# Performance work log

Hardware: AMD Instinct MI355X
Metric: run time of the kernel (lower is better)

## Reference

```python
import jax, jax.numpy as jnp
import numpy as np

B, D, H, Z, E = 2048, 1024, 1024, 256, 64


def setup_inputs() -> dict:
    key = jax.random.key(0)
    ks = jax.random.split(key, 16)
    s = lambda k, shape, std=0.02: jax.random.normal(k, shape, dtype=jnp.float32) * std
    return {
        "x": jax.random.normal(ks[0], (B, D), dtype=jnp.float32),
        "h0": jax.random.normal(ks[1], (B, H), dtype=jnp.float32),
        "c0": jax.random.normal(ks[2], (B, H), dtype=jnp.float32),
        "hhat0": jax.random.normal(ks[3], (B, Z), dtype=jnp.float32),
        "chat0": jax.random.normal(ks[4], (B, Z), dtype=jnp.float32),
        "hweight": s(ks[5], (Z + H + D, 4 * Z)),
        "hbias": jnp.zeros((4 * Z,), jnp.float32),
        "zweight_h": s(ks[6], (Z, 4 * E), 0.01),
        "zweight_x": s(ks[7], (Z, 4 * E), 0.01),
        "zweight_b": s(ks[8], (Z, 4 * E), 0.01),
        "zbias_h": jnp.ones((4 * E,), jnp.float32),
        "zbias_x": jnp.ones((4 * E,), jnp.float32),
        # stacked in gate order (i, g, f, o), matching the torch cat order
        "dweight_h": jnp.full((4, E, H), 0.1 / E, jnp.float32),
        "dweight_x": jnp.full((4, E, H), 0.1 / E, jnp.float32),
        "dweight_b": s(ks[9], (4, E, H), 0.01),
        "weight": s(ks[10], (H + D, 4 * H)),
        "bias": jnp.zeros((4 * H,), jnp.float32),
    }


def reference(x, h0, c0, hhat0, chat0, hweight, hbias,
              zweight_h, zweight_x, zweight_b, zbias_h, zbias_x,
              dweight_h, dweight_x, dweight_b, weight, bias):
    # ---- hyper LSTM cell ----
    hcat = jnp.concatenate([hhat0, h0, x], axis=1)                 # [B, Z+H+D]
    hg = hcat @ hweight + hbias                                    # [B, 4Z]
    i_h, g_h, f_h, o_h = jnp.split(hg, 4, axis=1)
    chat1 = jax.nn.sigmoid(f_h) * chat0 + jax.nn.sigmoid(i_h) * jnp.tanh(g_h)
    hhat1 = jax.nn.sigmoid(o_h) * jnp.tanh(chat1)                  # [B, Z]

    # ---- embeddings z (gate order i, g, f, o) ----
    z_h = (hhat1 @ zweight_h + zbias_h).reshape(-1, 4, E)          # [B,4,E]
    z_x = (hhat1 @ zweight_x + zbias_x).reshape(-1, 4, E)
    z_b = (hhat1 @ zweight_b).reshape(-1, 4, E)

    # ---- per-gate modulation vectors d_y* : [B,4,H] -> [B,4H] ----
    d_yh = jnp.einsum('bge,geh->bgh', z_h, dweight_h).reshape(-1, 4 * H)
    d_yx = jnp.einsum('bge,geh->bgh', z_x, dweight_x).reshape(-1, 4 * H)
    d_yb = jnp.einsum('bge,geh->bgh', z_b, dweight_b).reshape(-1, 4 * H)

    # ---- main LSTM with hypernetwork modulation ----
    gates = jnp.concatenate([h0, x], axis=1) @ weight              # [B, 4H]
    gates = gates * d_yh * d_yx + d_yb + bias
    i_g, g_g, f_g, o_g = jnp.split(gates, 4, axis=1)
    c1 = jax.nn.sigmoid(f_g) * c0 + jax.nn.sigmoid(i_g) * jnp.tanh(g_g)
    h1 = jax.nn.sigmoid(o_g) * jnp.tanh(c1)
    return (h1, c1, hhat1, chat1)
```

## Files before the change

### kernel.cpp

```cpp
#include <hip/hip_runtime.h>
#include <hip/hip_bf16.h>
#include <math.h>


typedef __attribute__((ext_vector_type(8))) short bf16x8;
typedef __attribute__((ext_vector_type(4))) float f32x4;
typedef unsigned short u16;

__device__ __forceinline__ u16 f2b(float f) {
  union { float f; unsigned u; } v; v.f = f;
  unsigned r = v.u + 0x7fffu + ((v.u >> 16) & 1u);
  return (u16)(r >> 16);
}
__device__ __forceinline__ float b2f(u16 b) {
  union { unsigned u; float f; } v; v.u = ((unsigned)b) << 16; return v.f;
}
__device__ __forceinline__ float sigm(float x) { return 1.f / (1.f + __expf(-x)); }

#define GLL16(gsrc, ldst)                                                      \
  __builtin_amdgcn_global_load_lds(                                            \
      (const __attribute__((address_space(1))) void*)(gsrc),                   \
      (__attribute__((address_space(3))) void*)(ldst), 16, 0, 0)

__global__ void k_prep(const float* __restrict__ hhat0, const float* __restrict__ h0,
                       const float* __restrict__ x, const float* __restrict__ weight,
                       const float* __restrict__ hweight,
                       const float* __restrict__ zw_h, const float* __restrict__ zw_x,
                       const float* __restrict__ zw_b, const float* __restrict__ dw_h,
                       const float* __restrict__ dw_x, const float* __restrict__ dw_b,
                       u16* __restrict__ hcatb, u16* __restrict__ bt,
                       u16* __restrict__ zwT, u16* __restrict__ dwT) {
  __shared__ float tile[32][66];
  int bid = blockIdx.x;
  const int t = threadIdx.x;
  if (bid < 4608) {
    int i = bid * 256 + t;
    int b = i / 576, c4 = i % 576;
    const float* src;
    if (c4 < 64)       src = hhat0 + (long)b * 256 + c4 * 4;
    else if (c4 < 320) src = h0 + (long)b * 1024 + (c4 - 64) * 4;
    else               src = x + (long)b * 1024 + (c4 - 320) * 4;
    float4 v = *(const float4*)src;
    ushort4 o = {f2b(v.x), f2b(v.y), f2b(v.z), f2b(v.w)};
    *(ushort4*)&hcatb[(long)b * 2304 + c4 * 4] = o;
    return;
  }
  bid -= 4608;
  if (bid < 5760) {
    const int n0 = (bid % 160) * 32, k0 = (bid / 160) * 64;
    if (n0 < 4096 && k0 < 256) return;
    const float* src; int C, sc0, sr0;
    if (n0 >= 4096) { src = hweight; C = 1024; sc0 = n0 - 4096; sr0 = k0; }
    else            { src = weight;  C = 4096; sc0 = n0;        sr0 = k0 - 256; }
    #pragma unroll
    for (int p = 0; p < 8; ++p) {
      int c = t & 31, r = (t >> 5) + 8 * p;
      tile[c][r] = src[(long)(sr0 + r) * C + sc0 + c];
    }
    __syncthreads();
    #pragma unroll
    for (int p = 0; p < 2; ++p) {
      int kc = t & 15, cl = (t >> 4) + 16 * p;
      ushort4 o = {f2b(tile[cl][4 * kc]), f2b(tile[cl][4 * kc + 1]),
                   f2b(tile[cl][4 * kc + 2]), f2b(tile[cl][4 * kc + 3])};
      *(ushort4*)&bt[(long)(n0 + cl) * 2304 + k0 + 4 * kc] = o;
    }
    return;
  }
  bid -= 5760;
  const int zi = bid >> 5, bx = bid & 31;
  const float* src; u16* dst; int R, C;
  if (zi < 3) {
    src = (zi == 0) ? zw_h : (zi == 1) ? zw_x : zw_b;
    dst = zwT + (long)zi * 65536; R = 256; C = 256;
  } else {
    int s = zi - 3, tt = s >> 2, g = s & 3;
    src = ((tt == 0) ? dw_h : (tt == 1) ? dw_x : dw_b) + (long)g * 65536;
    dst = dwT + (long)s * 65536; R = 64; C = 1024;
  }
  const int nct = C / 32;
  const int c0 = (bx % nct) * 32, r0 = (bx / nct) * 64;
  #pragma unroll
  for (int p = 0; p < 8; ++p) {
    int c = t & 31, r = (t >> 5) + 8 * p;
    tile[c][r] = src[(long)(r0 + r) * C + c0 + c];
  }
  __syncthreads();
  #pragma unroll
  for (int p = 0; p < 2; ++p) {
    int kc = t & 15, cl = (t >> 4) + 16 * p;
    ushort4 o = {f2b(tile[cl][4 * kc]), f2b(tile[cl][4 * kc + 1]),
                 f2b(tile[cl][4 * kc + 2]), f2b(tile[cl][4 * kc + 3])};
    *(ushort4*)&dst[(long)(c0 + cl) * R + r0 + 4 * kc] = o;
  }
}

__global__ __launch_bounds__(512, 4)
void k_gemm_main(const u16* __restrict__ A, const u16* __restrict__ Bt,
                 float* __restrict__ hgbuf, u16* __restrict__ grawb) {
  constexpr int K = 2304, BK = 64;
  __shared__ __align__(16) u16 sA[128 * BK];
  __shared__ __align__(16) u16 sB[128 * BK];
  const int m0 = blockIdx.y * 128, n0 = blockIdx.x * 128;
  const int kstart = (n0 < 4096) ? 256 : 0;
  const int tid = threadIdx.x, wave = tid >> 6, lane = tid & 63;
  const int quad = lane >> 4, lrow = lane & 15;
  const int wm = (wave >> 2) * 64, wn = (wave & 3) * 32;

  const int la = tid * 16;
  const int rowa = la >> 7, qa = (((la >> 4) & 7) - rowa) & 7;
  const int lb = 8192 + tid * 16;
  const int rowb = lb >> 7, qb = (((lb >> 4) & 7) - rowb) & 7;
  const long aoff0 = ((long)(m0 + rowa) * K + qa * 8) * 2;
  const long aoff1 = ((long)(m0 + rowb) * K + qb * 8) * 2;
  const long boff0 = ((long)(n0 + rowa) * K + qa * 8) * 2;
  const long boff1 = ((long)(n0 + rowb) * K + qb * 8) * 2;

  const f32x4 vz = {0.f, 0.f, 0.f, 0.f};
  f32x4 acc[4][2];
  #pragma unroll
  for (int i = 0; i < 4; ++i)
    #pragma unroll
    for (int j = 0; j < 2; ++j) acc[i][j] = vz;

  for (int k0 = kstart; k0 < K; k0 += BK) {
    GLL16((const char*)A + aoff0 + (long)k0 * 2, (char*)sA + wave * 1024);
    GLL16((const char*)A + aoff1 + (long)k0 * 2, (char*)sA + 8192 + wave * 1024);
    GLL16((const char*)Bt + boff0 + (long)k0 * 2, (char*)sB + wave * 1024);
    GLL16((const char*)Bt + boff1 + (long)k0 * 2, (char*)sB + 8192 + wave * 1024);
    __syncthreads();

    bf16x8 af[4][2], bf[2][2];
    #pragma unroll
    for (int i = 0; i < 4; ++i) {
      int row = wm + i * 16 + lrow;
      const char* base = (const char*)sA + row * 128;
      af[i][0] = *(const bf16x8*)(base + (((quad + row) & 7) << 4));
      af[i][1] = *(const bf16x8*)(base + (((4 + quad + row) & 7) << 4));
    }
    #pragma unroll
    for (int j = 0; j < 2; ++j) {
      int row = wn + j * 16 + lrow;
      const char* base = (const char*)sB + row * 128;
      bf[j][0] = *(const bf16x8*)(base + (((quad + row) & 7) << 4));
      bf[j][1] = *(const bf16x8*)(base + (((4 + quad + row) & 7) << 4));
    }
    #pragma unroll
    for (int kk = 0; kk < 2; ++kk)
      #pragma unroll
      for (int i = 0; i < 4; ++i)
        #pragma unroll
        for (int j = 0; j < 2; ++j)
          acc[i][j] = __builtin_amdgcn_mfma_f32_16x16x32_bf16(af[i][kk], bf[j][kk], acc[i][j], 0, 0, 0);
    __syncthreads();
  }

  #pragma unroll
  for (int i = 0; i < 4; ++i) {
    #pragma unroll
    for (int j = 0; j < 2; ++j) {
      #pragma unroll
      for (int r = 0; r < 4; ++r) {
        int row = m0 + wm + i * 16 + quad * 4 + r;
        int col = n0 + wn + j * 16 + lrow;
        float v = acc[i][j][r];
        if (col < 4096) grawb[(long)row * 4096 + col] = f2b(v);
        else            hgbuf[(long)row * 1024 + (col - 4096)] = v;
      }
    }
  }
}

__global__ __launch_bounds__(256, 2)
void k_gemm_z(const u16* __restrict__ A, const u16* __restrict__ Bt,
              const float* __restrict__ zbh, const float* __restrict__ zbx,
              u16* __restrict__ zbout) {
  constexpr int K = 256, BK = 32;
  __shared__ __align__(16) u16 sA[64 * BK];
  __shared__ __align__(16) u16 sB[128 * BK];
  const int m0 = blockIdx.y * 64, n0 = blockIdx.x * 128;
  const int tid = threadIdx.x, wave = tid >> 6, lane = tid & 63;
  const int quad = lane >> 4, lrow = lane & 15;
  const int wm = (wave >> 1) * 32, wn = (wave & 1) * 64;

  const int sl = tid * 16;
  const int arow = sl >> 6;
  const int aq = (((sl & 63) >> 4) - (arow >> 1)) & 3;
  const long aoff = ((long)(m0 + arow) * K) * 2 + aq * 16;

  const f32x4 vz = {0.f, 0.f, 0.f, 0.f};
  f32x4 acc[2][4];
  #pragma unroll
  for (int i = 0; i < 2; ++i)
    #pragma unroll
    for (int j = 0; j < 4; ++j) acc[i][j] = vz;

  for (int k0 = 0; k0 < K; k0 += BK) {
    GLL16((const char*)A + aoff + (long)k0 * 2, (char*)sA + wave * 1024);
    #pragma unroll
    for (int c = 0; c < 2; ++c) {
      int l = c * 4096 + sl;
      int row = l >> 6;
      int q = (((l & 63) >> 4) - (row >> 1)) & 3;
      const char* g = (const char*)Bt + ((long)(n0 + row) * K + k0) * 2 + q * 16;
      GLL16(g, (char*)sB + c * 4096 + wave * 1024);
    }
    __syncthreads();
    bf16x8 af[2], bf[4];
    #pragma unroll
    for (int i = 0; i < 2; ++i) {
      int row = wm + i * 16 + lrow;
      af[i] = *(const bf16x8*)((const char*)sA + row * 64 + (((quad + (row >> 1)) & 3) << 4));
    }
    #pragma unroll
    for (int j = 0; j < 4; ++j) {
      int row = wn + j * 16 + lrow;
      bf[j] = *(const bf16x8*)((const char*)sB + row * 64 + (((quad + (row >> 1)) & 3) << 4));
    }
    #pragma unroll
    for (int i = 0; i < 2; ++i)
      #pragma unroll
      for (int j = 0; j < 4; ++j)
        acc[i][j] = __builtin_amdgcn_mfma_f32_16x16x32_bf16(af[i], bf[j], acc[i][j], 0, 0, 0);
    __syncthreads();
  }
  #pragma unroll
  for (int i = 0; i < 2; ++i) {
    #pragma unroll
    for (int j = 0; j < 4; ++j) {
      #pragma unroll
      for (int r = 0; r < 4; ++r) {
        int row = m0 + wm + i * 16 + quad * 4 + r;
        int col = n0 + wn + j * 16 + lrow;
        float v = acc[i][j][r] + ((col < 256) ? zbh[col] : (col < 512) ? zbx[col - 256] : 0.f);
        zbout[(long)row * 768 + col] = f2b(v);
      }
    }
  }
}

__global__ void k_hyper_act(const float* __restrict__ hgbuf, const float* __restrict__ hbias,
                            const float* __restrict__ chat0,
                            float* __restrict__ chat1, float* __restrict__ hhat1,
                            u16* __restrict__ hhat1b) {
  int idx = blockIdx.x * 256 + threadIdx.x;
  int b = idx >> 8, zc = idx & 255;
  const float* row = hgbuf + (long)b * 1024;
  float ih = row[zc] + hbias[zc];
  float gh = row[256 + zc] + hbias[256 + zc];
  float fh = row[512 + zc] + hbias[512 + zc];
  float oh = row[768 + zc] + hbias[768 + zc];
  float c = sigm(fh) * chat0[idx] + sigm(ih) * tanhf(gh);
  float h = sigm(oh) * tanhf(c);
  chat1[idx] = c;
  hhat1[idx] = h;
  hhat1b[idx] = f2b(h);
}

__global__ __launch_bounds__(256, 2)
void k_dmod_lstm(const u16* __restrict__ z, const u16* __restrict__ dwT,
                 const u16* __restrict__ grawb, const float* __restrict__ bias,
                 const float* __restrict__ c0, float* __restrict__ h1,
                 float* __restrict__ c1) {
  __shared__ __align__(16) u16 sZ[64 * 192];
  __shared__ __align__(16) u16 sW[3 * 64 * 64];
  const int m0 = blockIdx.y * 64;
  const int hc0 = blockIdx.x * 64;
  const int tid = threadIdx.x, wave = tid >> 6, lane = tid & 63;
  const int quad = lane >> 4, lrow = lane & 15;
  const int wm = (wave >> 1) * 32, wn = (wave & 1) * 32;
  const f32x4 vz4 = {0.f, 0.f, 0.f, 0.f};

  f32x4 pcar[2][2];
  f32x4 ccar[2][2];

  #pragma unroll
  for (int g = 0; g < 4; ++g) {
    #pragma unroll
    for (int c = 0; c < 6; ++c) {
      int l = c * 4096 + tid * 16;
      int ci = l >> 4, row = ci / 24, p = ci - row * 24;
      int q = p + 72 - row; q -= (q / 24) * 24;
      int tt = q >> 3, e16 = q & 7;
      const char* gz = (const char*)z + (long)(m0 + row) * 1536 + tt * 512 + g * 128 + e16 * 16;
      GLL16(gz, (char*)sZ + c * 4096 + wave * 1024);
      int t2 = l >> 13, rw = (l & 8191) >> 7, p2 = (l >> 4) & 7;
      int q2 = (p2 - rw) & 7;
      const char* gw = (const char*)dwT + (long)((t2 * 4 + g) * 1024 + hc0 + rw) * 128 + q2 * 16;
      GLL16(gw, (char*)sW + c * 4096 + wave * 1024);
    }
    __syncthreads();
    f32x4 aH[2][2], aX[2][2], aB[2][2];
    #pragma unroll
    for (int i = 0; i < 2; ++i)
      #pragma unroll
      for (int j = 0; j < 2; ++j) { aH[i][j] = vz4; aX[i][j] = vz4; aB[i][j] = vz4; }
    #pragma unroll
    for (int kk = 0; kk < 2; ++kk) {
      bf16x8 za[3][2], wb[3][2];
      #pragma unroll
      for (int t = 0; t < 3; ++t) {
        #pragma unroll
        for (int i = 0; i < 2; ++i) {
          int row = wm + i * 16 + lrow;
          int q0 = t * 8 + kk * 4 + quad;
          int ph = q0 + row; ph -= (ph / 24) * 24;
          za[t][i] = *(const bf16x8*)((const char*)sZ + row * 384 + ph * 16);
        }
        #pragma unroll
        for (int j = 0; j < 2; ++j) {
          int row = wn + j * 16 + lrow;
          int q0 = kk * 4 + quad;
          int ph = (q0 + row) & 7;
          wb[t][j] = *(const bf16x8*)((const char*)sW + t * 8192 + row * 128 + ph * 16);
        }
      }
      #pragma unroll
      for (int i = 0; i < 2; ++i)
        #pragma unroll
        for (int j = 0; j < 2; ++j) {
          aH[i][j] = __builtin_amdgcn_mfma_f32_16x16x32_bf16(za[0][i], wb[0][j], aH[i][j], 0, 0, 0);
          aX[i][j] = __builtin_amdgcn_mfma_f32_16x16x32_bf16(za[1][i], wb[1][j], aX[i][j], 0, 0, 0);
          aB[i][j] = __builtin_amdgcn_mfma_f32_16x16x32_bf16(za[2][i], wb[2][j], aB[i][j], 0, 0, 0);
        }
    }
    __syncthreads();
    #pragma unroll
    for (int i = 0; i < 2; ++i) {
      #pragma unroll
      for (int j = 0; j < 2; ++j) {
        #pragma unroll
        for (int r = 0; r < 4; ++r) {
          int row = m0 + wm + i * 16 + quad * 4 + r;
          int col = wn + j * 16 + lrow;
          float gr = b2f(grawb[(long)row * 4096 + g * 1024 + hc0 + col]);
          float v = gr * aH[i][j][r] * aX[i][j][r] + aB[i][j][r] + bias[g * 1024 + hc0 + col];
          long idx = (long)row * 1024 + hc0 + col;
          if (g == 0) pcar[i][j][r] = sigm(v);
          else if (g == 1) pcar[i][j][r] *= tanhf(v);
          else if (g == 2) {
            float cc = sigm(v) * c0[idx] + pcar[i][j][r];
            ccar[i][j][r] = cc;
            c1[idx] = cc;
          } else {
            h1[idx] = sigm(v) * tanhf(ccar[i][j][r]);
          }
        }
      }
    }
  }
}


extern "C" void kernel_launch(void* const* d_in, const int* in_sizes, int n_in,
                              void* d_out, int out_size, void* d_ws, size_t ws_size,
                              hipStream_t stream) {
  const float* x      = (const float*)d_in[0];
  const float* h0     = (const float*)d_in[1];
  const float* c0     = (const float*)d_in[2];
  const float* hhat0  = (const float*)d_in[3];
  const float* chat0  = (const float*)d_in[4];
  const float* hweight= (const float*)d_in[5];
  const float* hbias  = (const float*)d_in[6];
  const float* zw_h   = (const float*)d_in[7];
  const float* zw_x   = (const float*)d_in[8];
  const float* zw_b   = (const float*)d_in[9];
  const float* zb_h   = (const float*)d_in[10];
  const float* zb_x   = (const float*)d_in[11];
  const float* dw_h   = (const float*)d_in[12];
  const float* dw_x   = (const float*)d_in[13];
  const float* dw_b   = (const float*)d_in[14];
  const float* weight = (const float*)d_in[15];
  const float* bias   = (const float*)d_in[16];
  float* out = (float*)d_out;

  char* w = (char*)d_ws;
  auto take = [&](size_t bytes) { char* p = w; w += (bytes + 255) & ~(size_t)255; return p; };
  u16*   hcatb  = (u16*)take(2048ull * 2304 * 2);
  u16*   btc    = (u16*)take(5120ull * 2304 * 2);
  u16*   zwT    = (u16*)take(768ull * 256 * 2);
  u16*   dwT    = (u16*)take(12ull * 1024 * 64 * 2);
  u16*   grawb  = (u16*)take(2048ull * 4096 * 2);
  float* hgbuf  = (float*)take(2048ull * 1024 * 4);
  u16*   hhat1b = (u16*)take(2048ull * 256 * 2);
  u16*   zb16   = (u16*)take(2048ull * 768 * 2);

  float* h1_o    = out;
  float* c1_o    = out + 2048 * 1024;
  float* hhat1_o = out + 2 * 2048 * 1024;
  float* chat1_o = out + 2 * 2048 * 1024 + 2048 * 256;

  k_prep<<<4608 + 5760 + 480, 256, 0, stream>>>(
      hhat0, h0, x, weight, hweight, zw_h, zw_x, zw_b, dw_h, dw_x, dw_b,
      hcatb, btc, zwT, dwT);

  k_gemm_main<<<dim3(40, 16), 512, 0, stream>>>(hcatb, btc, hgbuf, grawb);

  k_hyper_act<<<2048, 256, 0, stream>>>(hgbuf, hbias, chat0, chat1_o, hhat1_o, hhat1b);

  k_gemm_z<<<dim3(6, 32), 256, 0, stream>>>(hhat1b, zwT, zb_h, zb_x, zb16);

  k_dmod_lstm<<<dim3(16, 32), 256, 0, stream>>>(zb16, dwT, grawb, bias, c0, h1_o, c1_o);
}
```

Before: 225.0 us.

## Fuse hyper-LSTM activation into main GEMM epilogue and remap block order per XCD

Reorders the hweight columns during prep so the four gates of each hyper unit sit in adjacent output columns. This lets the main GEMM epilogue compute chat1/hhat1 directly with lane shuffles, and the separate activation kernel and its fp32 intermediate buffer are removed. The GEMM grid is also flattened with an XCD-aware block remap to improve L2 locality. The dmod kernel now stages its grawb tile into LDS via async global-to-LDS loads instead of scattered global reads. The cost is extra shuffles and redundant transcendental work in the epilogue, plus more LDS use in the dmod kernel.

```diff
diff --git a/kernel.cpp b/kernel.cpp
--- a/kernel.cpp
+++ b/kernel.cpp
@@ -49,9 +49,10 @@
   if (bid < 5760) {
     const int n0 = (bid % 160) * 32, k0 = (bid / 160) * 64;
     if (n0 < 4096 && k0 < 256) return;
+    const int isH = (n0 >= 4096);
     const float* src; int C, sc0, sr0;
-    if (n0 >= 4096) { src = hweight; C = 1024; sc0 = n0 - 4096; sr0 = k0; }
-    else            { src = weight;  C = 4096; sc0 = n0;        sr0 = k0 - 256; }
+    if (isH) { src = hweight; C = 1024; sc0 = n0 - 4096; sr0 = k0; }
+    else     { src = weight;  C = 4096; sc0 = n0;        sr0 = k0 - 256; }
     #pragma unroll
     for (int p = 0; p < 8; ++p) {
       int c = t & 31, r = (t >> 5) + 8 * p;
@@ -61,9 +62,12 @@
     #pragma unroll
     for (int p = 0; p < 2; ++p) {
       int kc = t & 15, cl = (t >> 4) + 16 * p;
+      int orow;
+      if (isH) { int u = sc0 + cl; orow = 4096 + ((u & 255) << 2) + (u >> 8); }
+      else     orow = n0 + cl;
       ushort4 o = {f2b(tile[cl][4 * kc]), f2b(tile[cl][4 * kc + 1]),
                    f2b(tile[cl][4 * kc + 2]), f2b(tile[cl][4 * kc + 3])};
-      *(ushort4*)&bt[(long)(n0 + cl) * 2304 + k0 + 4 * kc] = o;
+      *(ushort4*)&bt[(long)orow * 2304 + k0 + 4 * kc] = o;
     }
     return;
   }
@@ -97,11 +101,17 @@
 
 __global__ __launch_bounds__(512, 4)
 void k_gemm_main(const u16* __restrict__ A, const u16* __restrict__ Bt,
-                 float* __restrict__ hgbuf, u16* __restrict__ grawb) {
+                 const float* __restrict__ hbias, const float* __restrict__ chat0,
+                 u16* __restrict__ grawb, float* __restrict__ chat1,
+                 float* __restrict__ hhat1, u16* __restrict__ hhat1b) {
   constexpr int K = 2304, BK = 64;
   __shared__ __align__(16) u16 sA[128 * BK];
   __shared__ __align__(16) u16 sB[128 * BK];
-  const int m0 = blockIdx.y * 128, n0 = blockIdx.x * 128;
+  const int bid = blockIdx.x;
+  const int xcd = bid & 7, ii = bid >> 3;
+  const int bx = (ii % 5) * 8 + xcd;
+  const int by = ii / 5;
+  const int m0 = by * 128, n0 = bx * 128;
   const int kstart = (n0 < 4096) ? 256 : 0;
   const int tid = threadIdx.x, wave = tid >> 6, lane = tid & 63;
   const int quad = lane >> 4, lrow = lane & 15;
@@ -155,17 +165,41 @@
     __syncthreads();
   }
 
-  #pragma unroll
-  for (int i = 0; i < 4; ++i) {
-    #pragma unroll
-    for (int j = 0; j < 2; ++j) {
-      #pragma unroll
-      for (int r = 0; r < 4; ++r) {
-        int row = m0 + wm + i * 16 + quad * 4 + r;
-        int col = n0 + wn + j * 16 + lrow;
-        float v = acc[i][j][r];
-        if (col < 4096) grawb[(long)row * 4096 + col] = f2b(v);
-        else            hgbuf[(long)row * 1024 + (col - 4096)] = v;
+  if (n0 < 4096) {
+    #pragma unroll
+    for (int i = 0; i < 4; ++i)
+      #pragma unroll
+      for (int j = 0; j < 2; ++j)
+        #pragma unroll
+        for (int r = 0; r < 4; ++r) {
+          int row = m0 + wm + i * 16 + quad * 4 + r;
+          int col = n0 + wn + j * 16 + lrow;
+          grawb[(long)row * 4096 + col] = f2b(acc[i][j][r]);
+        }
+  } else {
+    const int ubase = (n0 - 4096) + wn;
+    #pragma unroll
+    for (int i = 0; i < 4; ++i) {
+      #pragma unroll
+      for (int j = 0; j < 2; ++j) {
+        int u = ubase + j * 16 + lrow;
+        int g = u & 3, z = u >> 2;
+        #pragma unroll
+        for (int r = 0; r < 4; ++r) {
+          int row = m0 + wm + i * 16 + quad * 4 + r;
+          float v = acc[i][j][r] + hbias[g * 256 + z];
+          float vi = __shfl(v, (lane & ~3) + 0);
+          float vg = __shfl(v, (lane & ~3) + 1);
+          float vf = __shfl(v, (lane & ~3) + 2);
+          float vo = __shfl(v, (lane & ~3) + 3);
+          float cc = sigm(vf) * chat0[(long)row * 256 + z] + sigm(vi) * tanhf(vg);
+          float hh = sigm(vo) * tanhf(cc);
+          if (g == 0) {
+            chat1[(long)row * 256 + z] = cc;
+            hhat1[(long)row * 256 + z] = hh;
+            hhat1b[(long)row * 256 + z] = f2b(hh);
+          }
+        }
       }
     }
   }
@@ -239,24 +273,6 @@
   }
 }
 
-__global__ void k_hyper_act(const float* __restrict__ hgbuf, const float* __restrict__ hbias,
-                            const float* __restrict__ chat0,
-                            float* __restrict__ chat1, float* __restrict__ hhat1,
-                            u16* __restrict__ hhat1b) {
-  int idx = blockIdx.x * 256 + threadIdx.x;
-  int b = idx >> 8, zc = idx & 255;
-  const float* row = hgbuf + (long)b * 1024;
-  float ih = row[zc] + hbias[zc];
-  float gh = row[256 + zc] + hbias[256 + zc];
-  float fh = row[512 + zc] + hbias[512 + zc];
-  float oh = row[768 + zc] + hbias[768 + zc];
-  float c = sigm(fh) * chat0[idx] + sigm(ih) * tanhf(gh);
-  float h = sigm(oh) * tanhf(c);
-  chat1[idx] = c;
-  hhat1[idx] = h;
-  hhat1b[idx] = f2b(h);
-}
-
 __global__ __launch_bounds__(256, 2)
 void k_dmod_lstm(const u16* __restrict__ z, const u16* __restrict__ dwT,
                  const u16* __restrict__ grawb, const float* __restrict__ bias,
@@ -264,6 +280,7 @@
                  float* __restrict__ c1) {
   __shared__ __align__(16) u16 sZ[64 * 192];
   __shared__ __align__(16) u16 sW[3 * 64 * 64];
+  __shared__ __align__(16) u16 sG[2][64 * 64];
   const int m0 = blockIdx.y * 64;
   const int hc0 = blockIdx.x * 64;
   const int tid = threadIdx.x, wave = tid >> 6, lane = tid & 63;
@@ -289,6 +306,13 @@
       const char* gw = (const char*)dwT + (long)((t2 * 4 + g) * 1024 + hc0 + rw) * 128 + q2 * 16;
       GLL16(gw, (char*)sW + c * 4096 + wave * 1024);
     }
+    #pragma unroll
+    for (int c = 0; c < 2; ++c) {
+      int l = c * 4096 + tid * 16;
+      int row = l >> 7, off = l & 127;
+      const char* gg = (const char*)grawb + ((long)(m0 + row) * 4096 + g * 1024 + hc0) * 2 + off;
+      GLL16(gg, (char*)sG[g & 1] + c * 4096 + wave * 1024);
+    }
     __syncthreads();
     f32x4 aH[2][2], aX[2][2], aB[2][2];
     #pragma unroll
@@ -325,15 +349,17 @@
         }
     }
     __syncthreads();
+    const u16* sGc = sG[g & 1];
     #pragma unroll
     for (int i = 0; i < 2; ++i) {
       #pragma unroll
       for (int j = 0; j < 2; ++j) {
         #pragma unroll
         for (int r = 0; r < 4; ++r) {
-          int row = m0 + wm + i * 16 + quad * 4 + r;
+          int rowl = wm + i * 16 + quad * 4 + r;
           int col = wn + j * 16 + lrow;
-          float gr = b2f(grawb[(long)row * 4096 + g * 1024 + hc0 + col]);
+          int row = m0 + rowl;
+          float gr = b2f(sGc[rowl * 64 + col]);
           float v = gr * aH[i][j][r] * aX[i][j][r] + aB[i][j][r] + bias[g * 1024 + hc0 + col];
           long idx = (long)row * 1024 + hc0 + col;
           if (g == 0) pcar[i][j][r] = sigm(v);
@@ -381,7 +407,6 @@
   u16*   zwT    = (u16*)take(768ull * 256 * 2);
   u16*   dwT    = (u16*)take(12ull * 1024 * 64 * 2);
   u16*   grawb  = (u16*)take(2048ull * 4096 * 2);
-  float* hgbuf  = (float*)take(2048ull * 1024 * 4);
   u16*   hhat1b = (u16*)take(2048ull * 256 * 2);
   u16*   zb16   = (u16*)take(2048ull * 768 * 2);
 
@@ -394,9 +419,8 @@
       hhat0, h0, x, weight, hweight, zw_h, zw_x, zw_b, dw_h, dw_x, dw_b,
       hcatb, btc, zwT, dwT);
 
-  k_gemm_main<<<dim3(40, 16), 512, 0, stream>>>(hcatb, btc, hgbuf, grawb);
-
-  k_hyper_act<<<2048, 256, 0, stream>>>(hgbuf, hbias, chat0, chat1_o, hhat1_o, hhat1b);
+  k_gemm_main<<<640, 512, 0, stream>>>(hcatb, btc, hbias, chat0,
+                                       grawb, chat1_o, hhat1_o, hhat1b);
 
   k_gemm_z<<<dim3(6, 32), 256, 0, stream>>>(hhat1b, zwT, zb_h, zb_x, zb16);
 
```

Result: slower. 233.9 us (+4.0%).
